# Kernel optimization log

Hardware: AMD Instinct MI355X
Metric: run time of the kernel (lower is better)

## Reference

```python
import jax, jax.numpy as jnp
import numpy as np

N, E = 100000, 1600000
F1, H1, H2 = 128, 128, 128


def setup_inputs() -> dict:
    key = jax.random.key(0)
    ks = jax.random.split(key, 8)
    x = jax.random.normal(ks[0], (N, F1), dtype=jnp.float32)
    edge_index = jax.random.randint(ks[1], (2, E), 0, N, dtype=jnp.int64)
    s1 = 1.0 / np.sqrt(F1)
    s2 = 1.0 / np.sqrt(H1)
    s3 = 1.0 / np.sqrt(H2)
    W1 = jax.random.uniform(ks[2], (F1, H1), jnp.float32, -s1, s1)
    b1 = jax.random.uniform(ks[3], (H1,), jnp.float32, -s1, s1)
    W2 = jax.random.uniform(ks[4], (H1, H2), jnp.float32, -s2, s2)
    b2 = jax.random.uniform(ks[5], (H2,), jnp.float32, -s2, s2)
    Wc = jax.random.uniform(ks[6], (H2, 1), jnp.float32, -s3, s3)
    bc = jax.random.uniform(ks[7], (1,), jnp.float32, -s3, s3)
    return {"x": x, "edge_index": edge_index, "W1": W1, "b1": b1,
            "W2": W2, "b2": b2, "Wc": Wc, "bc": bc}


def _gcn_conv(h, W, b, row, col, norm, n):
    # linear transform then degree-normalized gather/scatter-add aggregation
    h = h @ W                                  # [N, out]
    msg = h[row] * norm[:, None]               # [E+N, out] gather + scale
    out = jax.ops.segment_sum(msg, col, num_segments=n)  # scatter-add
    return out + b


def reference(x, edge_index, W1, b1, W2, b2, Wc, bc):
    n = x.shape[0]
    loops = jnp.arange(n, dtype=edge_index.dtype)
    row = jnp.concatenate([edge_index[0], loops])  # sources (with self-loops)
    col = jnp.concatenate([edge_index[1], loops])  # targets (with self-loops)
    deg = jax.ops.segment_sum(jnp.ones_like(col, dtype=x.dtype), col,
                              num_segments=n)
    dinv = jnp.where(deg > 0, jax.lax.rsqrt(deg), 0.0)
    norm = dinv[row] * dinv[col]                   # symmetric normalization

    h = jnp.tanh(_gcn_conv(x, W1, b1, row, col, norm, n))
    h = jnp.tanh(_gcn_conv(h, W2, b2, row, col, norm, n))
    logits = (h @ Wc + bc)[:, 0]                   # [N]
    return jax.nn.softmax(logits)                  # softmax over all nodes
```

## Files before the change

kernel.cpp:

```cpp
#include <hip/hip_runtime.h>
#include <hip/hip_fp16.h>


#define BSHIFT 9
#define BSPAN  512
#define PCHUNK 4096
#define LCAP   12288

typedef _Float16 half8 __attribute__((ext_vector_type(8)));
typedef float floatx4 __attribute__((ext_vector_type(4)));

__device__ inline void fmix2(float& a0, float& a1, unsigned int h2) {
    asm("v_fma_mix_f32 %0, %1, 1.0, %0 op_sel:[0,0,0] op_sel_hi:[1,0,0]" : "+v"(a0) : "v"(h2));
    asm("v_fma_mix_f32 %0, %1, 1.0, %0 op_sel:[1,0,0] op_sel_hi:[1,0,0]" : "+v"(a1) : "v"(h2));
}
__device__ inline void fmix_acc8(float* acc, uint4 v) {
    fmix2(acc[0], acc[1], v.x);
    fmix2(acc[2], acc[3], v.y);
    fmix2(acc[4], acc[5], v.z);
    fmix2(acc[6], acc[7], v.w);
}

__device__ inline float tanh_fast(float x) {
    float e = __expf(2.0f * x);
    return 1.0f - 2.0f * __builtin_amdgcn_rcpf(e + 1.0f);
}

__global__ __launch_bounds__(256) void hist_buckets(const int* __restrict__ col, int E,
                                                    int* __restrict__ bucketCnt) {
    __shared__ int h[256];
    h[threadIdx.x] = 0;
    __syncthreads();
    for (int e = blockIdx.x * 256 + threadIdx.x; e < E; e += gridDim.x * 256)
        atomicAdd(&h[col[e] >> BSHIFT], 1);
    __syncthreads();
    int v = h[threadIdx.x];
    if (v) atomicAdd(&bucketCnt[threadIdx.x], v);
}

__global__ void scan_buckets(const int* __restrict__ cnt, int* __restrict__ bucketPtr,
                             int* __restrict__ cursor, int NB, int E) {
    __shared__ int s[256];
    int t = threadIdx.x;
    int v = (t < NB) ? cnt[t] : 0;
    s[t] = v;
    __syncthreads();
    for (int d = 1; d < 256; d <<= 1) {
        int x = (t >= d) ? s[t - d] : 0;
        __syncthreads();
        s[t] += x;
        __syncthreads();
    }
    if (t < NB) {
        int p = s[t] - v;
        bucketPtr[t] = p;
        cursor[t] = p;
    }
    if (t == 0) bucketPtr[NB] = E;
}

__global__ __launch_bounds__(256) void partition_edges(const int* __restrict__ row,
                                                       const int* __restrict__ col, int E,
                                                       int* __restrict__ cursor,
                                                       unsigned int* __restrict__ pairs) {
    __shared__ int hist[256], sscan[256], gdelta[256], hcur[256];
    __shared__ uint2 stage[PCHUNK];
    int t = threadIdx.x;
    int base = blockIdx.x * PCHUNK;
    int cnt = min(PCHUNK, E - base);
    hist[t] = 0;
    __syncthreads();
    uint2 v[16];
    int b_[16];
#pragma unroll
    for (int k = 0; k < 16; k++) {
        int idx = t + k * 256;
        if (idx < cnt) {
            int c = col[base + idx], r = row[base + idx];
            v[k] = make_uint2((unsigned)c, (unsigned)r);
            b_[k] = c >> BSHIFT;
            atomicAdd(&hist[b_[k]], 1);
        } else b_[k] = -1;
    }
    __syncthreads();
    int hv = hist[t];
    sscan[t] = hv;
    __syncthreads();
    for (int d = 1; d < 256; d <<= 1) {
        int x = (t >= d) ? sscan[t - d] : 0;
        __syncthreads();
        sscan[t] += x;
        __syncthreads();
    }
    int excl = sscan[t] - hv;
    if (hv > 0) {
        int g = atomicAdd(&cursor[t], hv);
        gdelta[t] = g - excl;
    }
    hcur[t] = excl;
    __syncthreads();
#pragma unroll
    for (int k = 0; k < 16; k++) {
        if (b_[k] >= 0) {
            int slot = atomicAdd(&hcur[b_[k]], 1);
            stage[slot] = v[k];
        }
    }
    __syncthreads();
    for (int i = t; i < cnt; i += 256) {
        uint2 p = stage[i];
        pairs[gdelta[p.x >> BSHIFT] + i] = (p.y << BSHIFT) | (p.x & (BSPAN - 1));
    }
}

__global__ __launch_bounds__(256) void build_bucket_csr(const unsigned int* __restrict__ pairs,
                                                        const int* __restrict__ bucketPtr,
                                                        int* __restrict__ rowptr,
                                                        float* __restrict__ dinv,
                                                        int* __restrict__ csr,
                                                        int n, int NB, int E) {
    __shared__ int hist[BSPAN];
    __shared__ int lptr[BSPAN];
    __shared__ int s[256];
    __shared__ int srcStage[LCAP];
    int b = blockIdx.x, t = threadIdx.x;
    int base = bucketPtr[b], cnt = bucketPtr[b + 1] - base;
    int node0 = b << BSHIFT;
    int nn = min(BSPAN, n - node0);
    hist[t] = 0; hist[t + 256] = 0;
    __syncthreads();
    for (int i = t; i < cnt; i += 256)
        atomicAdd(&hist[pairs[base + i] & (BSPAN - 1)], 1);
    __syncthreads();
    int a0 = hist[2 * t], a1 = hist[2 * t + 1];
    int sum = a0 + a1;
    s[t] = sum;
    __syncthreads();
    for (int d = 1; d < 256; d <<= 1) {
        int x = (t >= d) ? s[t - d] : 0;
        __syncthreads();
        s[t] += x;
        __syncthreads();
    }
    int excl = s[t] - sum;
    lptr[2 * t] = excl;
    lptr[2 * t + 1] = excl + a0;
    __syncthreads();
    for (int lc = t; lc < nn; lc += 256) {
        rowptr[node0 + lc] = base + lptr[lc];
        dinv[node0 + lc] = rsqrtf((float)(hist[lc] + 1));
    }
    if (b == NB - 1 && t == 0) rowptr[n] = E;
    __syncthreads();
    hist[t] = 0; hist[t + 256] = 0;
    __syncthreads();
    bool inLds = (cnt <= LCAP);
    for (int i = t; i < cnt; i += 256) {
        unsigned int p = pairs[base + i];
        int lc = p & (BSPAN - 1);
        int rank = atomicAdd(&hist[lc], 1);
        int slot = lptr[lc] + rank;
        if (inLds) srcStage[slot] = (int)(p >> BSHIFT);
        else csr[base + slot] = (int)(p >> BSHIFT);
    }
    __syncthreads();
    if (inLds)
        for (int i = t; i < cnt; i += 256) csr[base + i] = srcStage[i];
}

__global__ __launch_bounds__(256) void prep_wfrags(const float* __restrict__ W1,
                                                   const float* __restrict__ W2,
                                                   uint4* __restrict__ F1,
                                                   uint4* __restrict__ F2) {
    int g = blockIdx.x * 256 + threadIdx.x;
    const float* W = (g < 2048) ? W1 : W2;
    uint4* F = (g < 2048) ? F1 : F2;
    int t = g & 2047;
    int lane = t & 63, ct = (t >> 6) & 7, ks = t >> 9;
    int col = ct * 16 + (lane & 15);
    int kb = ks * 32 + (lane >> 4) * 8;
    half8 v;
#pragma unroll
    for (int j = 0; j < 8; j++) v[j] = (_Float16)W[(kb + j) * 128 + col];
    F[t] = __builtin_bit_cast(uint4, v);
}

template <bool HALF_IN>
__global__ __launch_bounds__(256) void gemm_mfma(const void* __restrict__ Ap,
                                                 const uint4* __restrict__ F,
                                                 const float* __restrict__ dinv,
                                                 unsigned short* __restrict__ C, int n) {
    int w = threadIdx.x >> 6, lane = threadIdx.x & 63;
    int r0 = blockIdx.x * 128 + w * 32;
    int rA0 = r0 + (lane & 15);
    int rA1 = rA0 + 16;
    int kc = lane >> 4;
    floatx4 acc[2][8] = {};

#pragma unroll
    for (int ks = 0; ks < 4; ks++) {
        half8 a0 = {}, a1 = {};
        if constexpr (HALF_IN) {
            const uint4* A4 = (const uint4*)Ap;
            if (rA0 < n) a0 = __builtin_bit_cast(half8, A4[(size_t)rA0 * 16 + ks * 4 + kc]);
            if (rA1 < n) a1 = __builtin_bit_cast(half8, A4[(size_t)rA1 * 16 + ks * 4 + kc]);
        } else {
            const float* Af = (const float*)Ap;
            if (rA0 < n) {
                const float4* p = (const float4*)&Af[(size_t)rA0 * 128 + ks * 32 + kc * 8];
                float4 u = p[0], v = p[1];
                a0[0] = (_Float16)u.x; a0[1] = (_Float16)u.y; a0[2] = (_Float16)u.z; a0[3] = (_Float16)u.w;
                a0[4] = (_Float16)v.x; a0[5] = (_Float16)v.y; a0[6] = (_Float16)v.z; a0[7] = (_Float16)v.w;
            }
            if (rA1 < n) {
                const float4* p = (const float4*)&Af[(size_t)rA1 * 128 + ks * 32 + kc * 8];
                float4 u = p[0], v = p[1];
                a1[0] = (_Float16)u.x; a1[1] = (_Float16)u.y; a1[2] = (_Float16)u.z; a1[3] = (_Float16)u.w;
                a1[4] = (_Float16)v.x; a1[5] = (_Float16)v.y; a1[6] = (_Float16)v.z; a1[7] = (_Float16)v.w;
            }
        }
        half8 b[8];
#pragma unroll
        for (int ct = 0; ct < 8; ct++)
            b[ct] = __builtin_bit_cast(half8, F[ks * 512 + ct * 64 + lane]);
#pragma unroll
        for (int ct = 0; ct < 8; ct++) {
            acc[0][ct] = __builtin_amdgcn_mfma_f32_16x16x32_f16(a0, b[ct], acc[0][ct], 0, 0, 0);
            acc[1][ct] = __builtin_amdgcn_mfma_f32_16x16x32_f16(a1, b[ct], acc[1][ct], 0, 0, 0);
        }
    }

#pragma unroll
    for (int rt = 0; rt < 2; rt++) {
        int rbase = r0 + rt * 16 + (lane >> 4) * 4;
#pragma unroll
        for (int reg = 0; reg < 4; reg++) {
            int r = rbase + reg;
            if (r < n) {
                float di = dinv[r];
#pragma unroll
                for (int ct = 0; ct < 8; ct++) {
                    _Float16 h = (_Float16)(acc[rt][ct][reg] * di);
                    C[(size_t)r * 128 + ct * 16 + (lane & 15)] =
                        __builtin_bit_cast(unsigned short, h);
                }
            }
        }
    }
}

__global__ __launch_bounds__(256) void aggregate(const uint4* __restrict__ T,
                                                 const int* __restrict__ csr,
                                                 const int* __restrict__ rowptr,
                                                 const float* __restrict__ dinv,
                                                 const float* __restrict__ bias,
                                                 unsigned int* __restrict__ Out, int n) {
    int node = (int)((blockIdx.x * 256 + threadIdx.x) >> 6);
    int lane = threadIdx.x & 63;
    if (node >= n) return;
    int grp = lane >> 4, m = lane & 15;

    float acc[8] = {};
    int beg = rowptr[node], end = rowptr[node + 1];
    int e = beg;
    while (e < end) {
        int take = min(end - e, 64);
        int myidx = (lane < take) ? csr[e + lane] : 0;
#pragma unroll 4
        for (int j = 0; j < take; j += 4) {
            int src = __shfl(myidx, j + grp);
            if (j + grp < take) {
                uint4 v = T[(size_t)src * 16 + m];
                fmix_acc8(acc, v);
            }
        }
        e += take;
    }
#pragma unroll
    for (int q = 0; q < 8; q++) {
        acc[q] += __shfl_xor(acc[q], 16);
        acc[q] += __shfl_xor(acc[q], 32);
    }

    int u = m * 4 + grp;
    float a0 = acc[2 * grp], a1 = acc[2 * grp + 1];
    unsigned int self = ((const unsigned int*)T)[(size_t)node * 64 + u];
    fmix2(a0, a1, self);
    float di = dinv[node];
    float2 b = *(const float2*)&bias[m * 8 + 2 * grp];
    float o0 = tanh_fast(a0 * di + b.x);
    float o1 = tanh_fast(a1 * di + b.y);
    Out[(size_t)node * 64 + u] = __builtin_bit_cast(unsigned int, __floats2half2_rn(o0, o1));
}

__global__ __launch_bounds__(256) void aggregate_logits(const uint4* __restrict__ T,
                                                        const int* __restrict__ csr,
                                                        const int* __restrict__ rowptr,
                                                        const float* __restrict__ dinv,
                                                        const float* __restrict__ bias,
                                                        const float* __restrict__ Wc,
                                                        const float* __restrict__ bc,
                                                        float* __restrict__ logits, int n) {
    int node = (int)((blockIdx.x * 256 + threadIdx.x) >> 6);
    int lane = threadIdx.x & 63;
    if (node >= n) return;
    int grp = lane >> 4, m = lane & 15;

    float acc[8] = {};
    int beg = rowptr[node], end = rowptr[node + 1];
    int e = beg;
    while (e < end) {
        int take = min(end - e, 64);
        int myidx = (lane < take) ? csr[e + lane] : 0;
#pragma unroll 4
        for (int j = 0; j < take; j += 4) {
            int src = __shfl(myidx, j + grp);
            if (j + grp < take) {
                uint4 v = T[(size_t)src * 16 + m];
                fmix_acc8(acc, v);
            }
        }
        e += take;
    }
#pragma unroll
    for (int q = 0; q < 8; q++) {
        acc[q] += __shfl_xor(acc[q], 16);
        acc[q] += __shfl_xor(acc[q], 32);
    }

    int u = m * 4 + grp;
    float a0 = acc[2 * grp], a1 = acc[2 * grp + 1];
    unsigned int self = ((const unsigned int*)T)[(size_t)node * 64 + u];
    fmix2(a0, a1, self);
    float di = dinv[node];
    float2 b = *(const float2*)&bias[m * 8 + 2 * grp];
    float2 w = *(const float2*)&Wc[m * 8 + 2 * grp];
    float d = tanh_fast(a0 * di + b.x) * w.x + tanh_fast(a1 * di + b.y) * w.y;
#pragma unroll
    for (int off = 1; off < 64; off <<= 1) d += __shfl_xor(d, off);
    if (lane == 0) logits[node] = d + bc[0];
}

__global__ __launch_bounds__(256) void maxpart(const float* __restrict__ logits, int n,
                                               float* __restrict__ partialMax,
                                               float* __restrict__ denom) {
    if (blockIdx.x == 0 && threadIdx.x == 0) *denom = 0.0f;
    __shared__ float s[256];
    float m = -3.4e38f;
    for (int i = blockIdx.x * 256 + threadIdx.x; i < n; i += 256 * 256)
        m = fmaxf(m, logits[i]);
    s[threadIdx.x] = m;
    __syncthreads();
    for (int d = 128; d; d >>= 1) {
        if (threadIdx.x < d) s[threadIdx.x] = fmaxf(s[threadIdx.x], s[threadIdx.x + d]);
        __syncthreads();
    }
    if (threadIdx.x == 0) partialMax[blockIdx.x] = s[0];
}

__global__ __launch_bounds__(256) void exp_kernel(const float* __restrict__ logits,
                                                  const float* __restrict__ partialMax,
                                                  float* __restrict__ outv,
                                                  float* __restrict__ denom, int n) {
    __shared__ float s[256];
    s[threadIdx.x] = partialMax[threadIdx.x];
    __syncthreads();
    for (int d = 128; d; d >>= 1) {
        if (threadIdx.x < d) s[threadIdx.x] = fmaxf(s[threadIdx.x], s[threadIdx.x + d]);
        __syncthreads();
    }
    float maxv = s[0];
    __syncthreads();
    int i = blockIdx.x * 256 + threadIdx.x;
    float e = 0.0f;
    if (i < n) {
        e = expf(logits[i] - maxv);
        outv[i] = e;
    }
    s[threadIdx.x] = e;
    __syncthreads();
    for (int d = 128; d; d >>= 1) {
        if (threadIdx.x < d) s[threadIdx.x] += s[threadIdx.x + d];
        __syncthreads();
    }
    if (threadIdx.x == 0) atomicAdd(denom, s[0]);
}

__global__ __launch_bounds__(256) void norm_kernel(float* __restrict__ out,
                                                   const float* __restrict__ denom, int n) {
    int i = blockIdx.x * 256 + threadIdx.x;
    if (i < n) out[i] = out[i] / (*denom);
}

extern "C" void kernel_launch(void* const* d_in, const int* in_sizes, int n_in,
                              void* d_out, int out_size, void* d_ws, size_t ws_size,
                              hipStream_t stream) {
    const float* x  = (const float*)d_in[0];
    const int*   ei = (const int*)d_in[1];
    const float* W1 = (const float*)d_in[2];
    const float* b1 = (const float*)d_in[3];
    const float* W2 = (const float*)d_in[4];
    const float* b2 = (const float*)d_in[5];
    const float* Wc = (const float*)d_in[6];
    const float* bc = (const float*)d_in[7];

    int n = in_sizes[0] / 128;
    int E = in_sizes[1] / 2;
    const int* row = ei;
    const int* col = ei + E;
    int NB = (n + BSPAN - 1) >> BSHIFT;

    char* ws = (char*)d_ws;
    size_t off = 0;
    auto alloc = [&](size_t bytes) -> void* {
        void* p = ws + off;
        off += (bytes + 255) & ~(size_t)255;
        return p;
    };
    uint4*  A        = (uint4*)alloc((size_t)n * 128 * 2);
    uint4*  B        = (uint4*)alloc((size_t)n * 128 * 2);
    unsigned int* pairs = (unsigned int*)alloc((size_t)E * 4);
    int*    csr      = (int*)alloc((size_t)E * 4);
    float*  dinv     = (float*)alloc((size_t)n * 4);
    int*    rowptr   = (int*)alloc((size_t)(n + 1) * 4);
    int*    bucketCnt= (int*)alloc(256 * 4);
    int*    bucketPtr= (int*)alloc(257 * 4);
    int*    cursor   = (int*)alloc(256 * 4);
    uint4*  F1       = (uint4*)alloc(2048 * 16);
    uint4*  F2       = (uint4*)alloc(2048 * 16);
    float*  logits   = (float*)alloc((size_t)n * 4);
    float*  pmax     = (float*)alloc(256 * 4);
    float*  denom    = (float*)alloc(4);

    int nbN = (n + 255) / 256;
    int nbW = (n + 3) / 4;
    int nbG = (n + 127) / 128;

    hipMemsetAsync(bucketCnt, 0, 256 * 4, stream);

    hist_buckets<<<512, 256, 0, stream>>>(col, E, bucketCnt);
    scan_buckets<<<1, 256, 0, stream>>>(bucketCnt, bucketPtr, cursor, NB, E);
    partition_edges<<<(E + PCHUNK - 1) / PCHUNK, 256, 0, stream>>>(row, col, E, cursor, pairs);
    prep_wfrags<<<16, 256, 0, stream>>>(W1, W2, F1, F2);
    build_bucket_csr<<<NB, 256, 0, stream>>>(pairs, bucketPtr, rowptr, dinv, csr, n, NB, E);

    gemm_mfma<false><<<nbG, 256, 0, stream>>>(x, F1, dinv, (unsigned short*)A, n);
    aggregate<<<nbW, 256, 0, stream>>>(A, csr, rowptr, dinv, b1, (unsigned int*)B, n);
    gemm_mfma<true><<<nbG, 256, 0, stream>>>(B, F2, dinv, (unsigned short*)A, n);
    aggregate_logits<<<nbW, 256, 0, stream>>>(A, csr, rowptr, dinv, b2, Wc, bc, logits, n);

    maxpart<<<256, 256, 0, stream>>>(logits, n, pmax, denom);
    exp_kernel<<<nbN, 256, 0, stream>>>(logits, pmax, (float*)d_out, denom, n);
    norm_kernel<<<nbN, 256, 0, stream>>>((float*)d_out, denom, n);
}
```

Before: 244.3 us.

## Store transformed features as FP8 to halve gather traffic in aggregation

The GEMM epilogue now writes the dinv-scaled transformed features as packed FP8 (128 bytes per node) instead of FP16, using a permuted column layout so each lane packs eight output columns. The aggregation kernels gather 8 uint4 chunks per neighbour with 8 neighbours in flight per wavefront, unpack them with the FP8-to-f32 converts, and remap dimensions when applying bias and Wc. The second-layer weight fragments are row-permuted so the FP16 hidden output stays consistent with that layout. The aim is to cut the bandwidth of the random gather over 1.7M edges, at the cost of FP8 rounding error in the messages and a more complex index mapping.

```diff
diff --git a/kernel.cpp b/kernel.cpp
--- a/kernel.cpp
+++ b/kernel.cpp
@@ -9,21 +9,22 @@
 
 typedef _Float16 half8 __attribute__((ext_vector_type(8)));
 typedef float floatx4 __attribute__((ext_vector_type(4)));
-
-__device__ inline void fmix2(float& a0, float& a1, unsigned int h2) {
-    asm("v_fma_mix_f32 %0, %1, 1.0, %0 op_sel:[0,0,0] op_sel_hi:[1,0,0]" : "+v"(a0) : "v"(h2));
-    asm("v_fma_mix_f32 %0, %1, 1.0, %0 op_sel:[1,0,0] op_sel_hi:[1,0,0]" : "+v"(a1) : "v"(h2));
-}
-__device__ inline void fmix_acc8(float* acc, uint4 v) {
-    fmix2(acc[0], acc[1], v.x);
-    fmix2(acc[2], acc[3], v.y);
-    fmix2(acc[4], acc[5], v.z);
-    fmix2(acc[6], acc[7], v.w);
-}
+typedef float floatx2 __attribute__((ext_vector_type(2)));
 
 __device__ inline float tanh_fast(float x) {
     float e = __expf(2.0f * x);
     return 1.0f - 2.0f * __builtin_amdgcn_rcpf(e + 1.0f);
+}
+
+__device__ inline void fp8_acc16(floatx2* acc, uint4 v) {
+    acc[0] += __builtin_amdgcn_cvt_pk_f32_fp8((int)v.x, false);
+    acc[1] += __builtin_amdgcn_cvt_pk_f32_fp8((int)v.x, true);
+    acc[2] += __builtin_amdgcn_cvt_pk_f32_fp8((int)v.y, false);
+    acc[3] += __builtin_amdgcn_cvt_pk_f32_fp8((int)v.y, true);
+    acc[4] += __builtin_amdgcn_cvt_pk_f32_fp8((int)v.z, false);
+    acc[5] += __builtin_amdgcn_cvt_pk_f32_fp8((int)v.z, true);
+    acc[6] += __builtin_amdgcn_cvt_pk_f32_fp8((int)v.w, false);
+    acc[7] += __builtin_amdgcn_cvt_pk_f32_fp8((int)v.w, true);
 }
 
 __global__ __launch_bounds__(256) void hist_buckets(const int* __restrict__ col, int E,
@@ -173,15 +174,20 @@
                                                    uint4* __restrict__ F1,
                                                    uint4* __restrict__ F2) {
     int g = blockIdx.x * 256 + threadIdx.x;
-    const float* W = (g < 2048) ? W1 : W2;
-    uint4* F = (g < 2048) ? F1 : F2;
+    bool second = (g >= 2048);
+    const float* W = second ? W2 : W1;
+    uint4* F = second ? F2 : F1;
     int t = g & 2047;
     int lane = t & 63, ct = (t >> 6) & 7, ks = t >> 9;
     int col = ct * 16 + (lane & 15);
     int kb = ks * 32 + (lane >> 4) * 8;
     half8 v;
 #pragma unroll
-    for (int j = 0; j < 8; j++) v[j] = (_Float16)W[(kb + j) * 128 + col];
+    for (int j = 0; j < 8; j++) {
+        int k = kb + j;
+        int krow = second ? (((k & 7) << 4) | (k >> 3)) : k;
+        v[j] = (_Float16)W[krow * 128 + col];
+    }
     F[t] = __builtin_bit_cast(uint4, v);
 }
 
@@ -189,7 +195,7 @@
 __global__ __launch_bounds__(256) void gemm_mfma(const void* __restrict__ Ap,
                                                  const uint4* __restrict__ F,
                                                  const float* __restrict__ dinv,
-                                                 unsigned short* __restrict__ C, int n) {
+                                                 unsigned char* __restrict__ T8, int n) {
     int w = threadIdx.x >> 6, lane = threadIdx.x & 63;
     int r0 = blockIdx.x * 128 + w * 32;
     int rA0 = r0 + (lane & 15);
@@ -230,6 +236,7 @@
         }
     }
 
+    int c = lane & 15;
 #pragma unroll
     for (int rt = 0; rt < 2; rt++) {
         int rbase = r0 + rt * 16 + (lane >> 4) * 4;
@@ -238,18 +245,20 @@
             int r = rbase + reg;
             if (r < n) {
                 float di = dinv[r];
-#pragma unroll
-                for (int ct = 0; ct < 8; ct++) {
-                    _Float16 h = (_Float16)(acc[rt][ct][reg] * di);
-                    C[(size_t)r * 128 + ct * 16 + (lane & 15)] =
-                        __builtin_bit_cast(unsigned short, h);
-                }
+                float vv[8];
+#pragma unroll
+                for (int ct = 0; ct < 8; ct++) vv[ct] = acc[rt][ct][reg] * di;
+                int d0 = __builtin_amdgcn_cvt_pk_fp8_f32(vv[0], vv[1], 0, false);
+                d0 = __builtin_amdgcn_cvt_pk_fp8_f32(vv[2], vv[3], d0, true);
+                int d1 = __builtin_amdgcn_cvt_pk_fp8_f32(vv[4], vv[5], 0, false);
+                d1 = __builtin_amdgcn_cvt_pk_fp8_f32(vv[6], vv[7], d1, true);
+                *(uint2*)(T8 + (size_t)r * 128 + c * 8) = make_uint2((unsigned)d0, (unsigned)d1);
             }
         }
     }
 }
 
-__global__ __launch_bounds__(256) void aggregate(const uint4* __restrict__ T,
+__global__ __launch_bounds__(256) void aggregate(const unsigned char* __restrict__ T8,
                                                  const int* __restrict__ csr,
                                                  const int* __restrict__ rowptr,
                                                  const float* __restrict__ dinv,
@@ -258,42 +267,44 @@
     int node = (int)((blockIdx.x * 256 + threadIdx.x) >> 6);
     int lane = threadIdx.x & 63;
     if (node >= n) return;
-    int grp = lane >> 4, m = lane & 15;
-
-    float acc[8] = {};
+    int grp = lane >> 3, m = lane & 7;
+    const uint4* T4 = (const uint4*)T8;
+
+    floatx2 acc[8] = {};
     int beg = rowptr[node], end = rowptr[node + 1];
     int e = beg;
     while (e < end) {
         int take = min(end - e, 64);
         int myidx = (lane < take) ? csr[e + lane] : 0;
-#pragma unroll 4
-        for (int j = 0; j < take; j += 4) {
+#pragma unroll 2
+        for (int j = 0; j < take; j += 8) {
             int src = __shfl(myidx, j + grp);
-            if (j + grp < take) {
-                uint4 v = T[(size_t)src * 16 + m];
-                fmix_acc8(acc, v);
-            }
+            if (j + grp < take) fp8_acc16(acc, T4[(size_t)src * 8 + m]);
         }
         e += take;
     }
-#pragma unroll
-    for (int q = 0; q < 8; q++) {
-        acc[q] += __shfl_xor(acc[q], 16);
-        acc[q] += __shfl_xor(acc[q], 32);
-    }
-
-    int u = m * 4 + grp;
-    float a0 = acc[2 * grp], a1 = acc[2 * grp + 1];
-    unsigned int self = ((const unsigned int*)T)[(size_t)node * 64 + u];
-    fmix2(a0, a1, self);
+    float* af = (float*)acc;
+#pragma unroll
+    for (int q = 0; q < 16; q++) {
+        af[q] += __shfl_xor(af[q], 8);
+        af[q] += __shfl_xor(af[q], 16);
+        af[q] += __shfl_xor(af[q], 32);
+    }
+
+    int q = m * 16 + 2 * grp;
+    int dim = ((q & 7) << 4) | (q >> 3);
+    unsigned short us = *(const unsigned short*)(T8 + (size_t)node * 128 + q);
+    floatx2 self = __builtin_amdgcn_cvt_pk_f32_fp8((int)us, false);
+    float a0 = acc[grp].x + self.x, a1 = acc[grp].y + self.y;
     float di = dinv[node];
-    float2 b = *(const float2*)&bias[m * 8 + 2 * grp];
-    float o0 = tanh_fast(a0 * di + b.x);
-    float o1 = tanh_fast(a1 * di + b.y);
-    Out[(size_t)node * 64 + u] = __builtin_bit_cast(unsigned int, __floats2half2_rn(o0, o1));
-}
-
-__global__ __launch_bounds__(256) void aggregate_logits(const uint4* __restrict__ T,
+    float b0 = bias[dim], b1 = bias[dim + 16];
+    float o0 = tanh_fast(a0 * di + b0);
+    float o1 = tanh_fast(a1 * di + b1);
+    Out[(size_t)node * 64 + (q >> 1)] =
+        __builtin_bit_cast(unsigned int, __floats2half2_rn(o0, o1));
+}
+
+__global__ __launch_bounds__(256) void aggregate_logits(const unsigned char* __restrict__ T8,
                                                         const int* __restrict__ csr,
                                                         const int* __restrict__ rowptr,
                                                         const float* __restrict__ dinv,
@@ -304,38 +315,39 @@
     int node = (int)((blockIdx.x * 256 + threadIdx.x) >> 6);
     int lane = threadIdx.x & 63;
     if (node >= n) return;
-    int grp = lane >> 4, m = lane & 15;
-
-    float acc[8] = {};
+    int grp = lane >> 3, m = lane & 7;
+    const uint4* T4 = (const uint4*)T8;
+
+    floatx2 acc[8] = {};
     int beg = rowptr[node], end = rowptr[node + 1];
     int e = beg;
     while (e < end) {
         int take = min(end - e, 64);
         int myidx = (lane < take) ? csr[e + lane] : 0;
-#pragma unroll 4
-        for (int j = 0; j < take; j += 4) {
+#pragma unroll 2
+        for (int j = 0; j < take; j += 8) {
             int src = __shfl(myidx, j + grp);
-            if (j + grp < take) {
-                uint4 v = T[(size_t)src * 16 + m];
-                fmix_acc8(acc, v);
-            }
+            if (j + grp < take) fp8_acc16(acc, T4[(size_t)src * 8 + m]);
         }
         e += take;
     }
-#pragma unroll
-    for (int q = 0; q < 8; q++) {
-        acc[q] += __shfl_xor(acc[q], 16);
-        acc[q] += __shfl_xor(acc[q], 32);
-    }
-
-    int u = m * 4 + grp;
-    float a0 = acc[2 * grp], a1 = acc[2 * grp + 1];
-    unsigned int self = ((const unsigned int*)T)[(size_t)node * 64 + u];
-    fmix2(a0, a1, self);
+    float* af = (float*)acc;
+#pragma unroll
+    for (int q = 0; q < 16; q++) {
+        af[q] += __shfl_xor(af[q], 8);
+        af[q] += __shfl_xor(af[q], 16);
+        af[q] += __shfl_xor(af[q], 32);
+    }
+
+    int q = m * 16 + 2 * grp;
+    int dim = ((q & 7) << 4) | (q >> 3);
+    unsigned short us = *(const unsigned short*)(T8 + (size_t)node * 128 + q);
+    floatx2 self = __builtin_amdgcn_cvt_pk_f32_fp8((int)us, false);
+    float a0 = acc[grp].x + self.x, a1 = acc[grp].y + self.y;
     float di = dinv[node];
-    float2 b = *(const float2*)&bias[m * 8 + 2 * grp];
-    float2 w = *(const float2*)&Wc[m * 8 + 2 * grp];
-    float d = tanh_fast(a0 * di + b.x) * w.x + tanh_fast(a1 * di + b.y) * w.y;
+    float b0 = bias[dim], b1 = bias[dim + 16];
+    float w0 = Wc[dim], w1 = Wc[dim + 16];
+    float d = tanh_fast(a0 * di + b0) * w0 + tanh_fast(a1 * di + b1) * w1;
 #pragma unroll
     for (int off = 1; off < 64; off <<= 1) d += __shfl_xor(d, off);
     if (lane == 0) logits[node] = d + bc[0];
@@ -417,8 +429,9 @@
         off += (bytes + 255) & ~(size_t)255;
         return p;
     };
-    uint4*  A        = (uint4*)alloc((size_t)n * 128 * 2);
-    uint4*  B        = (uint4*)alloc((size_t)n * 128 * 2);
+    unsigned char* T1 = (unsigned char*)alloc((size_t)n * 128);
+    unsigned char* T2 = (unsigned char*)alloc((size_t)n * 128);
+    unsigned int*  H1 = (unsigned int*)alloc((size_t)n * 128 * 2);
     unsigned int* pairs = (unsigned int*)alloc((size_t)E * 4);
     int*    csr      = (int*)alloc((size_t)E * 4);
     float*  dinv     = (float*)alloc((size_t)n * 4);
@@ -444,10 +457,10 @@
     prep_wfrags<<<16, 256, 0, stream>>>(W1, W2, F1, F2);
     build_bucket_csr<<<NB, 256, 0, stream>>>(pairs, bucketPtr, rowptr, dinv, csr, n, NB, E);
 
-    gemm_mfma<false><<<nbG, 256, 0, stream>>>(x, F1, dinv, (unsigned short*)A, n);
-    aggregate<<<nbW, 256, 0, stream>>>(A, csr, rowptr, dinv, b1, (unsigned int*)B, n);
-    gemm_mfma<true><<<nbG, 256, 0, stream>>>(B, F2, dinv, (unsigned short*)A, n);
-    aggregate_logits<<<nbW, 256, 0, stream>>>(A, csr, rowptr, dinv, b2, Wc, bc, logits, n);
+    gemm_mfma<false><<<nbG, 256, 0, stream>>>(x, F1, dinv, T1, n);
+    aggregate<<<nbW, 256, 0, stream>>>(T1, csr, rowptr, dinv, b1, H1, n);
+    gemm_mfma<true><<<nbG, 256, 0, stream>>>(H1, F2, dinv, T2, n);
+    aggregate_logits<<<nbW, 256, 0, stream>>>(T2, csr, rowptr, dinv, b2, Wc, bc, logits, n);
 
     maxpart<<<256, 256, 0, stream>>>(logits, n, pmax, denom);
     exp_kernel<<<nbN, 256, 0, stream>>>(logits, pmax, (float*)d_out, denom, n);
```

After: 235.0 us. 1.04x faster.
